# Performance work log

Hardware: AMD Instinct MI355X
Metric: run time of the kernel (lower is better)

Reference implementation:

```python
import jax, jax.numpy as jnp
import numpy as np

T, H, N, Q, C = 65536, 768, 32768, 32768, 10
MAX_LEN = 16  # max span length


def _make_spans(key, n):
    k1, k2 = jax.random.split(key)
    starts = jax.random.randint(k1, (n,), 0, T - MAX_LEN)
    lengths = jax.random.randint(k2, (n,), 1, MAX_LEN + 1)
    return jnp.stack([starts, starts + lengths], axis=1)  # [start, end)


def setup_inputs() -> dict:
    key = jax.random.key(0)
    ks = jax.random.split(key, 6)
    token_emb = jax.random.normal(ks[0], (T, H), dtype=jnp.float32)
    spans_support = _make_spans(ks[1], N)
    labels = jax.random.randint(ks[2], (N,), 0, C)
    spans_query = _make_spans(ks[3], Q)
    W_proj = jax.random.normal(ks[4], (3 * H, H), dtype=jnp.float32) * (1.0 / np.sqrt(3 * H))
    b_proj = jnp.zeros((H,), dtype=jnp.float32)
    return dict(token_emb=token_emb, spans_support=spans_support, labels=labels,
                spans_query=spans_query, W_proj=W_proj, b_proj=b_proj, n_classes=C)


def _span_embed(token_emb, spans, W, b):
    # token_emb: (T, H); spans: (n, 2) [start, end)
    s = spans[:, 0]
    e = spans[:, 1]
    # exclusive-prefix-sum trick turns per-span mean pooling into two gathers
    zero = jnp.zeros((1, token_emb.shape[1]), token_emb.dtype)
    csum = jnp.concatenate([zero, jnp.cumsum(token_emb, axis=0)], axis=0)  # (T+1, H)
    h_mean = (csum[e] - csum[s]) / (e - s).astype(token_emb.dtype)[:, None]
    feat = jnp.concatenate([token_emb[s], token_emb[e - 1], h_mean], axis=-1)  # (n, 3H)
    return jax.nn.gelu(feat @ W + b, approximate=False)  # torch nn.GELU default = erf


def _l2norm(x, eps=1e-12):
    # matches torch F.normalize: x / max(||x||, eps)
    return x / jnp.maximum(jnp.linalg.norm(x, axis=-1, keepdims=True), eps)


def reference(token_emb, spans_support, labels, spans_query, W_proj, b_proj, n_classes):
    sup = _span_embed(token_emb, spans_support, W_proj, b_proj)  # (N, H)
    qry = _span_embed(token_emb, spans_query, W_proj, b_proj)    # (Q, H)
    # prototypes = per-class mean; empty classes fall back to global mean
    sums = jax.ops.segment_sum(sup, labels, num_segments=n_classes)           # (C, H)
    counts = jax.ops.segment_sum(jnp.ones((sup.shape[0],), sup.dtype), labels,
                                 num_segments=n_classes)                       # (C,)
    gmean = sup.mean(axis=0)
    protos = jnp.where(counts[:, None] > 0,
                       sums / jnp.maximum(counts, 1.0)[:, None],
                       gmean[None, :])
    # cosine metric + constant NONE logit of 0.5
    sim = _l2norm(qry) @ _l2norm(protos).T                                     # (Q, C)
    none_logit = jnp.full((qry.shape[0], 1), 0.5, dtype=qry.dtype)
    return jnp.concatenate([sim, none_logit], axis=-1)                         # (Q, C+1)
```

## Files before the change

kernel.cpp:

```cpp
#include <hip/hip_runtime.h>
#include <stdint.h>

#define H_DIM 768
#define N_SUP 32768
#define Q_QRY 32768
#define C_CLS 10
#define M_TOT 65536
#define KG 768
#define NG 2304
#define NT 12

typedef __bf16 bf16x8 __attribute__((ext_vector_type(8)));
typedef float f32x4 __attribute__((ext_vector_type(4)));
typedef __attribute__((address_space(3))) void lds_void;
typedef const __attribute__((address_space(1))) void g_void;

__device__ __forceinline__ ushort f2bf(float f) {
  union { float f; uint32_t u; } v; v.f = f;
  uint32_t r = (v.u + 0x7FFFu + ((v.u >> 16) & 1u)) >> 16;
  return (ushort)r;
}
__device__ __forceinline__ float bf2f(ushort h) {
  union { uint32_t u; float f; } v; v.u = ((uint32_t)h) << 16; return v.f;
}
__device__ __forceinline__ float gelu_f(float x) {
  return 0.5f * x * (1.0f + erff(x * 0.70710678118654752f));
}

__global__ void cvt_kernel(const float* __restrict__ te, ushort* __restrict__ tb) {
  size_t i = (((size_t)blockIdx.x * 256) + threadIdx.x) * 8;
  float4 v0 = *(const float4*)(te + i);
  float4 v1 = *(const float4*)(te + i + 4);
  ushort4 o0, o1;
  o0.x = f2bf(v0.x); o0.y = f2bf(v0.y); o0.z = f2bf(v0.z); o0.w = f2bf(v0.w);
  o1.x = f2bf(v1.x); o1.y = f2bf(v1.y); o1.z = f2bf(v1.z); o1.w = f2bf(v1.w);
  *(ushort4*)(tb + i) = o0;
  *(ushort4*)(tb + i + 4) = o1;
}

__global__ void wt2_kernel(const float* __restrict__ W, ushort* __restrict__ Bt) {
  int idx = blockIdx.x * 256 + threadIdx.x;
  int n = idx / KG, k = idx - n * KG;
  int blk = n / H_DIM;
  int c = n - blk * H_DIM;
  Bt[idx] = f2bf(W[(size_t)(blk * H_DIM + k) * H_DIM + c]);
}

__global__ __launch_bounds__(512, 2) void gemm8(const ushort* __restrict__ A,
                                                const ushort* __restrict__ Bt,
                                                ushort* __restrict__ C) {
  __shared__ ushort lds[65536];
  char* ldsc = (char*)lds;

  int orig = blockIdx.x;
  int wg = (orig & 7) * 288 + (orig >> 3);
  int rowT = wg / 9, colT = wg - rowT * 9;
  int m0 = rowT * 256, n0 = colT * 256;

  int tid = threadIdx.x;
  int lane = tid & 63, wave = tid >> 6;
  int wr = wave >> 2, wc = wave & 3;
  int l15 = lane & 15, l4 = lane >> 4;

  int row0 = tid >> 2;
  int ss = (tid & 3) ^ ((row0 >> 1) & 3);
  size_t eA0 = (size_t)(m0 + row0) * KG + ss * 8;
  size_t eA1 = (size_t)(m0 + row0 + 128) * KG + ss * 8;
  size_t eB0 = (size_t)(n0 + row0) * KG + ss * 8;
  size_t eB1 = (size_t)(n0 + row0 + 128) * KG + ss * 8;

  int aoff[8], boff[4];
#pragma unroll
  for (int m = 0; m < 8; ++m) {
    int r = wr * 128 + m * 16 + l15;
    aoff[m] = r * 64 + ((l4 ^ ((r >> 1) & 3)) << 4);
  }
#pragma unroll
  for (int n = 0; n < 4; ++n) {
    int r = wc * 64 + n * 16 + l15;
    boff[n] = r * 64 + ((l4 ^ ((r >> 1) & 3)) << 4);
  }

  f32x4 acc[8][4];
#pragma unroll
  for (int m = 0; m < 8; ++m)
#pragma unroll
    for (int n = 0; n < 4; ++n) acc[m][n] = (f32x4){0.f, 0.f, 0.f, 0.f};

#define SLOT_A(kh, db) (ldsc + ((kh) * 2 + (db)) * 16384)
#define SLOT_B(kh, db) (ldsc + 65536 + ((kh) * 2 + (db)) * 16384)
#define STAGE_A(tk, kh, db) do { \
    char* _d = SLOT_A(kh, db) + wave * 1024; \
    size_t _k = (size_t)(tk) * 64 + (kh) * 32; \
    __builtin_amdgcn_global_load_lds((g_void*)(A + eA0 + _k), (lds_void*)_d, 16, 0, 0); \
    __builtin_amdgcn_global_load_lds((g_void*)(A + eA1 + _k), (lds_void*)(_d + 8192), 16, 0, 0); \
  } while (0)
#define STAGE_B(tk, kh, db) do { \
    char* _d = SLOT_B(kh, db) + wave * 1024; \
    size_t _k = (size_t)(tk) * 64 + (kh) * 32; \
    __builtin_amdgcn_global_load_lds((g_void*)(Bt + eB0 + _k), (lds_void*)_d, 16, 0, 0); \
    __builtin_amdgcn_global_load_lds((g_void*)(Bt + eB1 + _k), (lds_void*)(_d + 8192), 16, 0, 0); \
  } while (0)
#define LDA4(base, o) do { _Pragma("unroll") for (int m = 0; m < 4; ++m) \
    af[m] = *reinterpret_cast<const bf16x8*>((base) + aoff[(o) + m]); } while (0)
#define LDB4(base) do { _Pragma("unroll") for (int n = 0; n < 4; ++n) \
    bf[n] = *reinterpret_cast<const bf16x8*>((base) + boff[n]); } while (0)
#define MFMA_BLOCK(MB) do { _Pragma("unroll") for (int m = 0; m < 4; ++m) \
  _Pragma("unroll") for (int n = 0; n < 4; ++n) \
    acc[(MB) + m][n] = __builtin_amdgcn_mfma_f32_16x16x32_bf16(af[m], bf[n], acc[(MB) + m][n], 0, 0, 0); \
  } while (0)
#define BARX() __builtin_amdgcn_s_barrier()
#define LGKM0() asm volatile("s_waitcnt lgkmcnt(0)" ::: "memory")
#define VM8() asm volatile("s_waitcnt vmcnt(8)" ::: "memory")

  STAGE_A(0, 0, 0); STAGE_B(0, 0, 0);
  STAGE_A(0, 1, 0); STAGE_B(0, 1, 0);
  STAGE_A(1, 0, 1); STAGE_B(1, 0, 1);
  VM8();
  BARX();

  bf16x8 af[4], bf[4];
  for (int t = 0; t < NT; ++t) {
    int d = t & 1, nd = d ^ 1;
    int tk1 = (t + 1 < NT) ? t + 1 : NT - 1;
    int tk2 = (t + 2 < NT) ? t + 2 : NT - 1;
    const char* Ak0 = SLOT_A(0, d); const char* Bk0 = SLOT_B(0, d);
    const char* Ak1 = SLOT_A(1, d); const char* Bk1 = SLOT_B(1, d);
    LDA4(Ak0, 0); LDB4(Bk0);
    STAGE_A(tk1, 1, nd);
    BARX(); LGKM0();
    __builtin_amdgcn_s_setprio(1); MFMA_BLOCK(0); __builtin_amdgcn_s_setprio(0);
    BARX();
    LDA4(Ak0, 4);
    STAGE_B(tk1, 1, nd);
    BARX(); LGKM0();
    __builtin_amdgcn_s_setprio(1); MFMA_BLOCK(4); __builtin_amdgcn_s_setprio(0);
    VM8(); BARX();
    LDA4(Ak1, 0); LDB4(Bk1);
    STAGE_A(tk2, 0, d);
    BARX(); LGKM0();
    __builtin_amdgcn_s_setprio(1); MFMA_BLOCK(0); __builtin_amdgcn_s_setprio(0);
    BARX();
    LDA4(Ak1, 4);
    STAGE_B(tk2, 0, d);
    BARX(); LGKM0();
    __builtin_amdgcn_s_setprio(1); MFMA_BLOCK(4); __builtin_amdgcn_s_setprio(0);
    VM8(); BARX();
  }
  asm volatile("s_waitcnt vmcnt(0)" ::: "memory");

#pragma unroll
  for (int m = 0; m < 8; ++m)
#pragma unroll
    for (int n = 0; n < 4; ++n) {
      int col = n0 + wc * 64 + n * 16 + l15;
      size_t rb = (size_t)(m0 + wr * 128 + m * 16 + l4 * 4) * NG + col;
#pragma unroll
      for (int v = 0; v < 4; ++v)
        C[rb + (size_t)v * NG] = f2bf(acc[m][n][v]);
    }
#undef SLOT_A
#undef SLOT_B
#undef STAGE_A
#undef STAGE_B
#undef LDA4
#undef LDB4
#undef MFMA_BLOCK
}

__global__ void combine_kernel(const ushort* __restrict__ PQR, const int* __restrict__ spS,
                               const int* __restrict__ spQ, const float* __restrict__ bias,
                               ushort* __restrict__ emb) {
  int wid = (int)((((size_t)blockIdx.x * blockDim.x) + threadIdx.x) >> 6);
  int lane = threadIdx.x & 63;
  if (wid >= M_TOT) return;
  int s, e;
  if (wid < N_SUP) { s = spS[2 * wid]; e = spS[2 * wid + 1]; }
  else             { int w = wid - N_SUP; s = spQ[2 * w]; e = spQ[2 * w + 1]; }
  int len = e - s;
  float inv = 1.0f / (float)len;

  float acc0[3][4], accr[3][4];
  const ushort* Pr = PQR + (size_t)s * NG;
  const ushort* Qr = PQR + (size_t)(e - 1) * NG + 768;
#pragma unroll
  for (int c = 0; c < 3; ++c) {
    int h = c * 256 + lane * 4;
    ushort4 p = *(const ushort4*)(Pr + h);
    ushort4 q = *(const ushort4*)(Qr + h);
    acc0[c][0] = bf2f(p.x) + bf2f(q.x);
    acc0[c][1] = bf2f(p.y) + bf2f(q.y);
    acc0[c][2] = bf2f(p.z) + bf2f(q.z);
    acc0[c][3] = bf2f(p.w) + bf2f(q.w);
    accr[c][0] = accr[c][1] = accr[c][2] = accr[c][3] = 0.f;
  }
  for (int r = s; r < e; ++r) {
    const ushort* Rr = PQR + (size_t)r * NG + 1536;
#pragma unroll
    for (int c = 0; c < 3; ++c) {
      int h = c * 256 + lane * 4;
      ushort4 rv = *(const ushort4*)(Rr + h);
      accr[c][0] += bf2f(rv.x); accr[c][1] += bf2f(rv.y);
      accr[c][2] += bf2f(rv.z); accr[c][3] += bf2f(rv.w);
    }
  }
  ushort* er = emb + (size_t)wid * H_DIM;
#pragma unroll
  for (int c = 0; c < 3; ++c) {
    int h = c * 256 + lane * 4;
    float4 bv = *(const float4*)(bias + h);
    ushort4 o;
    o.x = f2bf(gelu_f(acc0[c][0] + accr[c][0] * inv + bv.x));
    o.y = f2bf(gelu_f(acc0[c][1] + accr[c][1] * inv + bv.y));
    o.z = f2bf(gelu_f(acc0[c][2] + accr[c][2] * inv + bv.z));
    o.w = f2bf(gelu_f(acc0[c][3] + accr[c][3] * inv + bv.w));
    *(ushort4*)(er + h) = o;
  }
}

__global__ void proto_accum(const ushort* __restrict__ supEmb, const int* __restrict__ labels,
                            float* __restrict__ pSum, float* __restrict__ pCnt) {
  __shared__ float ls[C_CLS * H_DIM];
  __shared__ int lc[C_CLS];
  int t = threadIdx.x;
  for (int i = t; i < C_CLS * H_DIM; i += 256) ls[i] = 0.f;
  if (t < C_CLS) lc[t] = 0;
  __syncthreads();
  int base = blockIdx.x * 128;
  for (int si = 0; si < 128; ++si) {
    int sp = base + si;
    int lab = labels[sp];
    const ushort* er = supEmb + (size_t)sp * H_DIM;
#pragma unroll
    for (int j = 0; j < 3; ++j) {
      int c = t + j * 256;
      ls[lab * H_DIM + c] += bf2f(er[c]);
    }
    if (t == 0) lc[lab]++;
  }
  __syncthreads();
  for (int i = t; i < C_CLS * H_DIM; i += 256) atomicAdd(&pSum[i], ls[i]);
  if (t < C_CLS) atomicAdd(&pCnt[t], (float)lc[t]);
}

__global__ void proto_norm(const float* __restrict__ pSum, const float* __restrict__ pCnt,
                           float* __restrict__ pN) {
  __shared__ float red[4];
  int t = threadIdx.x, lane = t & 63, wave = t >> 6;
  for (int c = 0; c < C_CLS; ++c) {
    float cnt = pCnt[c];
    float x[3];
#pragma unroll
    for (int j = 0; j < 3; ++j) {
      int h = t + j * 256;
      float v;
      if (cnt > 0.5f) v = pSum[c * H_DIM + h] / cnt;
      else {
        float gs = 0.f;
        for (int cc = 0; cc < C_CLS; ++cc) gs += pSum[cc * H_DIM + h];
        v = gs / (float)N_SUP;
      }
      x[j] = v;
    }
    float ss = x[0] * x[0] + x[1] * x[1] + x[2] * x[2];
#pragma unroll
    for (int o = 32; o; o >>= 1) ss += __shfl_xor(ss, o);
    if (lane == 0) red[wave] = ss;
    __syncthreads();
    float tot = red[0] + red[1] + red[2] + red[3];
    float inv = 1.0f / fmaxf(sqrtf(tot), 1e-12f);
#pragma unroll
    for (int j = 0; j < 3; ++j) pN[c * H_DIM + t + j * 256] = x[j] * inv;
    __syncthreads();
  }
}

__global__ void sim_kernel(const ushort* __restrict__ emb, const float* __restrict__ pN,
                           float* __restrict__ out) {
  __shared__ float lp[C_CLS * H_DIM];
  int t = threadIdx.x;
  for (int i = t; i < C_CLS * H_DIM; i += 256) lp[i] = pN[i];
  __syncthreads();
  int lane = t & 63, wave = t >> 6;
  for (int row = blockIdx.x * 4 + wave; row < Q_QRY; row += gridDim.x * 4) {
    const ushort* qr = emb + (size_t)(N_SUP + row) * H_DIM;
    float dot[C_CLS] = {0, 0, 0, 0, 0, 0, 0, 0, 0, 0};
    float sq = 0.f;
#pragma unroll
    for (int j = 0; j < 12; ++j) {
      float v = bf2f(qr[lane + 64 * j]);
      sq += v * v;
#pragma unroll
      for (int p = 0; p < C_CLS; ++p) dot[p] += v * lp[p * H_DIM + lane + 64 * j];
    }
#pragma unroll
    for (int o = 32; o; o >>= 1) {
      sq += __shfl_xor(sq, o);
#pragma unroll
      for (int p = 0; p < C_CLS; ++p) dot[p] += __shfl_xor(dot[p], o);
    }
    if (lane == 0) {
      float inv = 1.0f / fmaxf(sqrtf(sq), 1e-12f);
      float* o = out + (size_t)row * (C_CLS + 1);
      o[0] = dot[0] * inv; o[1] = dot[1] * inv; o[2] = dot[2] * inv;
      o[3] = dot[3] * inv; o[4] = dot[4] * inv; o[5] = dot[5] * inv;
      o[6] = dot[6] * inv; o[7] = dot[7] * inv; o[8] = dot[8] * inv;
      o[9] = dot[9] * inv; o[10] = 0.5f;
    }
  }
}

extern "C" void kernel_launch(void* const* d_in, const int* in_sizes, int n_in,
                              void* d_out, int out_size, void* d_ws, size_t ws_size,
                              hipStream_t stream) {
  const float* token_emb = (const float*)d_in[0];
  const int*   spansS    = (const int*)d_in[1];
  const int*   labels    = (const int*)d_in[2];
  const int*   spansQ    = (const int*)d_in[3];
  const float* W         = (const float*)d_in[4];
  const float* b         = (const float*)d_in[5];
  float* out = (float*)d_out;

  char* ws = (char*)d_ws;
  size_t pqrB = (size_t)M_TOT * NG * 2;
  size_t embB = (size_t)M_TOT * H_DIM * 2;
  size_t wtB  = (size_t)NG * KG * 2;
  ushort* PQR  = (ushort*)ws;
  ushort* tebf = (ushort*)(ws + pqrB);
  ushort* emb  = tebf;
  ushort* Bt   = (ushort*)(ws + pqrB + embB);
  float*  pSum = (float*)(ws + pqrB + embB + wtB);
  float*  pCnt = pSum + C_CLS * H_DIM;
  float*  pN   = pCnt + 64;

  hipMemsetAsync(pSum, 0, (C_CLS * H_DIM + 64) * sizeof(float), stream);
  cvt_kernel<<<24576, 256, 0, stream>>>(token_emb, tebf);
  wt2_kernel<<<6912, 256, 0, stream>>>(W, Bt);
  gemm8<<<2304, 512, 0, stream>>>(tebf, Bt, PQR);
  combine_kernel<<<16384, 256, 0, stream>>>(PQR, spansS, spansQ, b, emb);
  proto_accum<<<N_SUP / 128, 256, 0, stream>>>(emb, labels, pSum, pCnt);
  proto_norm<<<1, 256, 0, stream>>>(pSum, pCnt, pN);
  sim_kernel<<<512, 256, 0, stream>>>(emb, pN, out);
}
```

Baseline: 630.1 us.

## Make GEMM persistent per row tile, looping over column tiles with cross-pass prefetch

```diff
diff --git a/kernel.cpp b/kernel.cpp
--- a/kernel.cpp
+++ b/kernel.cpp
@@ -9,6 +9,7 @@
 #define KG 768
 #define NG 2304
 #define NT 12
+#define NPASS 9
 
 typedef __bf16 bf16x8 __attribute__((ext_vector_type(8)));
 typedef float f32x4 __attribute__((ext_vector_type(4)));
@@ -46,16 +47,13 @@
   Bt[idx] = f2bf(W[(size_t)(blk * H_DIM + k) * H_DIM + c]);
 }
 
-__global__ __launch_bounds__(512, 2) void gemm8(const ushort* __restrict__ A,
-                                                const ushort* __restrict__ Bt,
-                                                ushort* __restrict__ C) {
+__global__ __launch_bounds__(512, 2) void gemm_p(const ushort* __restrict__ A,
+                                                 const ushort* __restrict__ Bt,
+                                                 ushort* __restrict__ C) {
   __shared__ ushort lds[65536];
   char* ldsc = (char*)lds;
 
-  int orig = blockIdx.x;
-  int wg = (orig & 7) * 288 + (orig >> 3);
-  int rowT = wg / 9, colT = wg - rowT * 9;
-  int m0 = rowT * 256, n0 = colT * 256;
+  int m0 = blockIdx.x * 256;
 
   int tid = threadIdx.x;
   int lane = tid & 63, wave = tid >> 6;
@@ -66,8 +64,8 @@
   int ss = (tid & 3) ^ ((row0 >> 1) & 3);
   size_t eA0 = (size_t)(m0 + row0) * KG + ss * 8;
   size_t eA1 = (size_t)(m0 + row0 + 128) * KG + ss * 8;
-  size_t eB0 = (size_t)(n0 + row0) * KG + ss * 8;
-  size_t eB1 = (size_t)(n0 + row0 + 128) * KG + ss * 8;
+  size_t eB0 = (size_t)row0 * KG + ss * 8;
+  size_t eB1 = (size_t)(row0 + 128) * KG + ss * 8;
 
   int aoff[8], boff[4];
 #pragma unroll
@@ -89,15 +87,15 @@
 
 #define SLOT_A(kh, db) (ldsc + ((kh) * 2 + (db)) * 16384)
 #define SLOT_B(kh, db) (ldsc + 65536 + ((kh) * 2 + (db)) * 16384)
-#define STAGE_A(tk, kh, db) do { \
+#define SA(kOff, kh, db) do { \
     char* _d = SLOT_A(kh, db) + wave * 1024; \
-    size_t _k = (size_t)(tk) * 64 + (kh) * 32; \
+    size_t _k = (size_t)(kOff) + (kh) * 32; \
     __builtin_amdgcn_global_load_lds((g_void*)(A + eA0 + _k), (lds_void*)_d, 16, 0, 0); \
     __builtin_amdgcn_global_load_lds((g_void*)(A + eA1 + _k), (lds_void*)(_d + 8192), 16, 0, 0); \
   } while (0)
-#define STAGE_B(tk, kh, db) do { \
+#define SB(cOff, kOff, kh, db) do { \
     char* _d = SLOT_B(kh, db) + wave * 1024; \
-    size_t _k = (size_t)(tk) * 64 + (kh) * 32; \
+    size_t _k = (size_t)(cOff) + (kOff) + (kh) * 32; \
     __builtin_amdgcn_global_load_lds((g_void*)(Bt + eB0 + _k), (lds_void*)_d, 16, 0, 0); \
     __builtin_amdgcn_global_load_lds((g_void*)(Bt + eB1 + _k), (lds_void*)(_d + 8192), 16, 0, 0); \
   } while (0)
@@ -107,62 +105,78 @@
     bf[n] = *reinterpret_cast<const bf16x8*>((base) + boff[n]); } while (0)
 #define MFMA_BLOCK(MB) do { _Pragma("unroll") for (int m = 0; m < 4; ++m) \
   _Pragma("unroll") for (int n = 0; n < 4; ++n) \
-    acc[(MB) + m][n] = __builtin_amdgcn_mfma_f32_16x16x32_bf16(af[m], bf[n], acc[(MB) + m][n], 0, 0, 0); \
+    acc[(MB) + m][n] = __builtin_amdgcn_mfma_f32_16x16x32_bf16(bf[n], af[m], acc[(MB) + m][n], 0, 0, 0); \
   } while (0)
 #define BARX() __builtin_amdgcn_s_barrier()
 #define LGKM0() asm volatile("s_waitcnt lgkmcnt(0)" ::: "memory")
-#define VM8() asm volatile("s_waitcnt vmcnt(8)" ::: "memory")
-
-  STAGE_A(0, 0, 0); STAGE_B(0, 0, 0);
-  STAGE_A(0, 1, 0); STAGE_B(0, 1, 0);
-  STAGE_A(1, 0, 1); STAGE_B(1, 0, 1);
-  VM8();
+#define VM4() asm volatile("s_waitcnt vmcnt(4)" ::: "memory")
+
+  SA(0, 0, 0);  SB(0, 0, 0, 0);
+  SA(0, 1, 0);  SB(0, 0, 1, 0);
+  SA(64, 0, 1); SB(0, 64, 0, 1);
+  VM4();
   BARX();
 
   bf16x8 af[4], bf[4];
-  for (int t = 0; t < NT; ++t) {
-    int d = t & 1, nd = d ^ 1;
-    int tk1 = (t + 1 < NT) ? t + 1 : NT - 1;
-    int tk2 = (t + 2 < NT) ? t + 2 : NT - 1;
-    const char* Ak0 = SLOT_A(0, d); const char* Bk0 = SLOT_B(0, d);
-    const char* Ak1 = SLOT_A(1, d); const char* Bk1 = SLOT_B(1, d);
-    LDA4(Ak0, 0); LDB4(Bk0);
-    STAGE_A(tk1, 1, nd);
-    BARX(); LGKM0();
-    __builtin_amdgcn_s_setprio(1); MFMA_BLOCK(0); __builtin_amdgcn_s_setprio(0);
-    BARX();
-    LDA4(Ak0, 4);
-    STAGE_B(tk1, 1, nd);
-    BARX(); LGKM0();
-    __builtin_amdgcn_s_setprio(1); MFMA_BLOCK(4); __builtin_amdgcn_s_setprio(0);
-    VM8(); BARX();
-    LDA4(Ak1, 0); LDB4(Bk1);
-    STAGE_A(tk2, 0, d);
-    BARX(); LGKM0();
-    __builtin_amdgcn_s_setprio(1); MFMA_BLOCK(0); __builtin_amdgcn_s_setprio(0);
-    BARX();
-    LDA4(Ak1, 4);
-    STAGE_B(tk2, 0, d);
-    BARX(); LGKM0();
-    __builtin_amdgcn_s_setprio(1); MFMA_BLOCK(4); __builtin_amdgcn_s_setprio(0);
-    VM8(); BARX();
+  for (int p = 0; p < NPASS; ++p) {
+    for (int t = 0; t < NT; ++t) {
+      int d = t & 1, nd = d ^ 1;
+      int tt1, ct1, tt2, ct2;
+      if (t < 11) { tt1 = t + 1; ct1 = p; } else { tt1 = 0; ct1 = p + 1; }
+      if (t < 10) { tt2 = t + 2; ct2 = p; } else { tt2 = t - 10; ct2 = p + 1; }
+      if (ct1 >= NPASS) { ct1 = NPASS - 1; tt1 = NT - 1; }
+      if (ct2 >= NPASS) { ct2 = NPASS - 1; tt2 = NT - 1; }
+      size_t cO1 = (size_t)ct1 * 256 * KG;
+      size_t cO2 = (size_t)ct2 * 256 * KG;
+      const char* Ak0 = SLOT_A(0, d); const char* Bk0 = SLOT_B(0, d);
+      const char* Ak1 = SLOT_A(1, d); const char* Bk1 = SLOT_B(1, d);
+      LDA4(Ak0, 0); LDB4(Bk0);
+      SA(tt1 * 64, 1, nd);
+      BARX(); LGKM0();
+      __builtin_amdgcn_s_setprio(1); MFMA_BLOCK(0); __builtin_amdgcn_s_setprio(0);
+      BARX();
+      LDA4(Ak0, 4);
+      SB(cO1, tt1 * 64, 1, nd);
+      BARX(); LGKM0();
+      __builtin_amdgcn_s_setprio(1); MFMA_BLOCK(4); __builtin_amdgcn_s_setprio(0);
+      BARX();
+      LDA4(Ak1, 0); LDB4(Bk1);
+      SA(tt2 * 64, 0, d);
+      BARX(); LGKM0();
+      __builtin_amdgcn_s_setprio(1); MFMA_BLOCK(0); __builtin_amdgcn_s_setprio(0);
+      BARX();
+      LDA4(Ak1, 4);
+      SB(cO2, tt2 * 64, 0, d);
+      BARX(); LGKM0();
+      __builtin_amdgcn_s_setprio(1); MFMA_BLOCK(4); __builtin_amdgcn_s_setprio(0);
+      VM4(); BARX();
+    }
+    {
+      int n0 = p * 256;
+#pragma unroll
+      for (int m = 0; m < 8; ++m) {
+        int row = m0 + wr * 128 + m * 16 + l15;
+#pragma unroll
+        for (int n = 0; n < 4; ++n) {
+          int col = n0 + wc * 64 + n * 16 + l4 * 4;
+          uint32_t lo, hi;
+          asm("v_cvt_pk_bf16_f32 %0, %1, %2" : "=v"(lo) : "v"(acc[m][n][0]), "v"(acc[m][n][1]));
+          asm("v_cvt_pk_bf16_f32 %0, %1, %2" : "=v"(hi) : "v"(acc[m][n][2]), "v"(acc[m][n][3]));
+          uint2 val; val.x = lo; val.y = hi;
+          *reinterpret_cast<uint2*>(C + (size_t)row * NG + col) = val;
+        }
+      }
+#pragma unroll
+      for (int m = 0; m < 8; ++m)
+#pragma unroll
+        for (int n = 0; n < 4; ++n) acc[m][n] = (f32x4){0.f, 0.f, 0.f, 0.f};
+    }
   }
   asm volatile("s_waitcnt vmcnt(0)" ::: "memory");
-
-#pragma unroll
-  for (int m = 0; m < 8; ++m)
-#pragma unroll
-    for (int n = 0; n < 4; ++n) {
-      int col = n0 + wc * 64 + n * 16 + l15;
-      size_t rb = (size_t)(m0 + wr * 128 + m * 16 + l4 * 4) * NG + col;
-#pragma unroll
-      for (int v = 0; v < 4; ++v)
-        C[rb + (size_t)v * NG] = f2bf(acc[m][n][v]);
-    }
 #undef SLOT_A
 #undef SLOT_B
-#undef STAGE_A
-#undef STAGE_B
+#undef SA
+#undef SB
 #undef LDA4
 #undef LDB4
 #undef MFMA_BLOCK
@@ -336,7 +350,7 @@
   hipMemsetAsync(pSum, 0, (C_CLS * H_DIM + 64) * sizeof(float), stream);
   cvt_kernel<<<24576, 256, 0, stream>>>(token_emb, tebf);
   wt2_kernel<<<6912, 256, 0, stream>>>(W, Bt);
-  gemm8<<<2304, 512, 0, stream>>>(tebf, Bt, PQR);
+  gemm_p<<<256, 512, 0, stream>>>(tebf, Bt, PQR);
   combine_kernel<<<16384, 256, 0, stream>>>(PQR, spansS, spansQ, b, emb);
   proto_accum<<<N_SUP / 128, 256, 0, stream>>>(emb, labels, pSum, pCnt);
   proto_norm<<<1, 256, 0, stream>>>(pSum, pCnt, pN);
```

Measured after the change: 673.3 us. 1.07x slower.

## Split GEMM output into P/Q/R planes, sort spans by start, restructure MFMA pipeline

Applied to the files above, without the earlier changes.

```diff
diff --git a/kernel.cpp b/kernel.cpp
--- a/kernel.cpp
+++ b/kernel.cpp
@@ -7,8 +7,8 @@
 #define C_CLS 10
 #define M_TOT 65536
 #define KG 768
-#define NG 2304
 #define NT 12
+#define NBUCK 1024
 
 typedef __bf16 bf16x8 __attribute__((ext_vector_type(8)));
 typedef float f32x4 __attribute__((ext_vector_type(4)));
@@ -46,16 +46,59 @@
   Bt[idx] = f2bf(W[(size_t)(blk * H_DIM + k) * H_DIM + c]);
 }
 
+__global__ void hist_kernel(const int* __restrict__ spS, const int* __restrict__ spQ,
+                            int* __restrict__ hist) {
+  __shared__ int lh[NBUCK];
+  int t = threadIdx.x;
+  for (int i = t; i < NBUCK; i += 256) lh[i] = 0;
+  __syncthreads();
+  for (int i = blockIdx.x * 256 + t; i < M_TOT; i += gridDim.x * 256) {
+    int s = (i < N_SUP) ? spS[2 * i] : spQ[2 * (i - N_SUP)];
+    atomicAdd(&lh[s >> 6], 1);
+  }
+  __syncthreads();
+  for (int i = t; i < NBUCK; i += 256) if (lh[i]) atomicAdd(&hist[i], lh[i]);
+}
+
+__global__ void prefix_kernel(const int* __restrict__ hist, int* __restrict__ cursor) {
+  __shared__ int tmp[NBUCK];
+  int t = threadIdx.x;
+  int v = hist[t];
+  tmp[t] = v;
+  __syncthreads();
+  for (int off = 1; off < NBUCK; off <<= 1) {
+    int add = (t >= off) ? tmp[t - off] : 0;
+    __syncthreads();
+    tmp[t] += add;
+    __syncthreads();
+  }
+  cursor[t] = tmp[t] - v;
+}
+
+__global__ void scatter_kernel(const int* __restrict__ spS, const int* __restrict__ spQ,
+                               int* __restrict__ cursor, int2* __restrict__ sorted) {
+  for (int i = blockIdx.x * 256 + threadIdx.x; i < M_TOT; i += gridDim.x * 256) {
+    int s, e;
+    if (i < N_SUP) { s = spS[2 * i]; e = spS[2 * i + 1]; }
+    else           { int w = i - N_SUP; s = spQ[2 * w]; e = spQ[2 * w + 1]; }
+    int pos = atomicAdd(&cursor[s >> 6], 1);
+    int2 rec; rec.x = s; rec.y = (i << 5) | (e - s);
+    sorted[pos] = rec;
+  }
+}
+
 __global__ __launch_bounds__(512, 2) void gemm8(const ushort* __restrict__ A,
                                                 const ushort* __restrict__ Bt,
-                                                ushort* __restrict__ C) {
+                                                ushort* __restrict__ Pp,
+                                                ushort* __restrict__ Qp,
+                                                ushort* __restrict__ Rp) {
   __shared__ ushort lds[65536];
   char* ldsc = (char*)lds;
 
   int orig = blockIdx.x;
   int wg = (orig & 7) * 288 + (orig >> 3);
   int rowT = wg / 9, colT = wg - rowT * 9;
-  int m0 = rowT * 256, n0 = colT * 256;
+  int m0 = rowT * 256;
 
   int tid = threadIdx.x;
   int lane = tid & 63, wave = tid >> 6;
@@ -66,8 +109,8 @@
   int ss = (tid & 3) ^ ((row0 >> 1) & 3);
   size_t eA0 = (size_t)(m0 + row0) * KG + ss * 8;
   size_t eA1 = (size_t)(m0 + row0 + 128) * KG + ss * 8;
-  size_t eB0 = (size_t)(n0 + row0) * KG + ss * 8;
-  size_t eB1 = (size_t)(n0 + row0 + 128) * KG + ss * 8;
+  size_t eB0 = (size_t)(colT * 256 + row0) * KG + ss * 8;
+  size_t eB1 = (size_t)(colT * 256 + row0 + 128) * KG + ss * 8;
 
   int aoff[8], boff[4];
 #pragma unroll
@@ -89,100 +132,95 @@
 
 #define SLOT_A(kh, db) (ldsc + ((kh) * 2 + (db)) * 16384)
 #define SLOT_B(kh, db) (ldsc + 65536 + ((kh) * 2 + (db)) * 16384)
-#define STAGE_A(tk, kh, db) do { \
-    char* _d = SLOT_A(kh, db) + wave * 1024; \
-    size_t _k = (size_t)(tk) * 64 + (kh) * 32; \
-    __builtin_amdgcn_global_load_lds((g_void*)(A + eA0 + _k), (lds_void*)_d, 16, 0, 0); \
-    __builtin_amdgcn_global_load_lds((g_void*)(A + eA1 + _k), (lds_void*)(_d + 8192), 16, 0, 0); \
+#define SAB(kOff, kh, db) do { \
+    char* _da = SLOT_A(kh, db) + wave * 1024; \
+    char* _db = SLOT_B(kh, db) + wave * 1024; \
+    size_t _k = (size_t)(kOff) + (kh) * 32; \
+    __builtin_amdgcn_global_load_lds((g_void*)(A + eA0 + _k), (lds_void*)_da, 16, 0, 0); \
+    __builtin_amdgcn_global_load_lds((g_void*)(A + eA1 + _k), (lds_void*)(_da + 8192), 16, 0, 0); \
+    __builtin_amdgcn_global_load_lds((g_void*)(Bt + eB0 + _k), (lds_void*)_db, 16, 0, 0); \
+    __builtin_amdgcn_global_load_lds((g_void*)(Bt + eB1 + _k), (lds_void*)(_db + 8192), 16, 0, 0); \
   } while (0)
-#define STAGE_B(tk, kh, db) do { \
-    char* _d = SLOT_B(kh, db) + wave * 1024; \
-    size_t _k = (size_t)(tk) * 64 + (kh) * 32; \
-    __builtin_amdgcn_global_load_lds((g_void*)(Bt + eB0 + _k), (lds_void*)_d, 16, 0, 0); \
-    __builtin_amdgcn_global_load_lds((g_void*)(Bt + eB1 + _k), (lds_void*)(_d + 8192), 16, 0, 0); \
-  } while (0)
-#define LDA4(base, o) do { _Pragma("unroll") for (int m = 0; m < 4; ++m) \
-    af[m] = *reinterpret_cast<const bf16x8*>((base) + aoff[(o) + m]); } while (0)
+#define LDA8(base) do { _Pragma("unroll") for (int m = 0; m < 8; ++m) \
+    af[m] = *reinterpret_cast<const bf16x8*>((base) + aoff[m]); } while (0)
 #define LDB4(base) do { _Pragma("unroll") for (int n = 0; n < 4; ++n) \
     bf[n] = *reinterpret_cast<const bf16x8*>((base) + boff[n]); } while (0)
-#define MFMA_BLOCK(MB) do { _Pragma("unroll") for (int m = 0; m < 4; ++m) \
+#define MFMA32() do { _Pragma("unroll") for (int m = 0; m < 8; ++m) \
   _Pragma("unroll") for (int n = 0; n < 4; ++n) \
-    acc[(MB) + m][n] = __builtin_amdgcn_mfma_f32_16x16x32_bf16(af[m], bf[n], acc[(MB) + m][n], 0, 0, 0); \
+    acc[m][n] = __builtin_amdgcn_mfma_f32_16x16x32_bf16(bf[n], af[m], acc[m][n], 0, 0, 0); \
   } while (0)
 #define BARX() __builtin_amdgcn_s_barrier()
 #define LGKM0() asm volatile("s_waitcnt lgkmcnt(0)" ::: "memory")
 #define VM8() asm volatile("s_waitcnt vmcnt(8)" ::: "memory")
 
-  STAGE_A(0, 0, 0); STAGE_B(0, 0, 0);
-  STAGE_A(0, 1, 0); STAGE_B(0, 1, 0);
-  STAGE_A(1, 0, 1); STAGE_B(1, 0, 1);
+  SAB(0, 0, 0);
+  SAB(0, 1, 0);
+  SAB(64, 0, 1);
   VM8();
   BARX();
 
-  bf16x8 af[4], bf[4];
+  bf16x8 af[8], bf[4];
   for (int t = 0; t < NT; ++t) {
     int d = t & 1, nd = d ^ 1;
-    int tk1 = (t + 1 < NT) ? t + 1 : NT - 1;
-    int tk2 = (t + 2 < NT) ? t + 2 : NT - 1;
-    const char* Ak0 = SLOT_A(0, d); const char* Bk0 = SLOT_B(0, d);
-    const char* Ak1 = SLOT_A(1, d); const char* Bk1 = SLOT_B(1, d);
-    LDA4(Ak0, 0); LDB4(Bk0);
-    STAGE_A(tk1, 1, nd);
+    int k1 = ((t + 1 < NT) ? t + 1 : NT - 1) * 64;
+    int k2 = ((t + 2 < NT) ? t + 2 : NT - 1) * 64;
+    LDA8(SLOT_A(0, d)); LDB4(SLOT_B(0, d));
+    SAB(k1, 1, nd);
     BARX(); LGKM0();
-    __builtin_amdgcn_s_setprio(1); MFMA_BLOCK(0); __builtin_amdgcn_s_setprio(0);
+    __builtin_amdgcn_s_setprio(1); MFMA32(); __builtin_amdgcn_s_setprio(0);
+    VM8();
     BARX();
-    LDA4(Ak0, 4);
-    STAGE_B(tk1, 1, nd);
+    LDA8(SLOT_A(1, d)); LDB4(SLOT_B(1, d));
+    SAB(k2, 0, d);
     BARX(); LGKM0();
-    __builtin_amdgcn_s_setprio(1); MFMA_BLOCK(4); __builtin_amdgcn_s_setprio(0);
-    VM8(); BARX();
-    LDA4(Ak1, 0); LDB4(Bk1);
-    STAGE_A(tk2, 0, d);
-    BARX(); LGKM0();
-    __builtin_amdgcn_s_setprio(1); MFMA_BLOCK(0); __builtin_amdgcn_s_setprio(0);
+    __builtin_amdgcn_s_setprio(1); MFMA32(); __builtin_amdgcn_s_setprio(0);
+    VM8();
     BARX();
-    LDA4(Ak1, 4);
-    STAGE_B(tk2, 0, d);
-    BARX(); LGKM0();
-    __builtin_amdgcn_s_setprio(1); MFMA_BLOCK(4); __builtin_amdgcn_s_setprio(0);
-    VM8(); BARX();
   }
   asm volatile("s_waitcnt vmcnt(0)" ::: "memory");
 
-#pragma unroll
-  for (int m = 0; m < 8; ++m)
-#pragma unroll
-    for (int n = 0; n < 4; ++n) {
-      int col = n0 + wc * 64 + n * 16 + l15;
-      size_t rb = (size_t)(m0 + wr * 128 + m * 16 + l4 * 4) * NG + col;
-#pragma unroll
-      for (int v = 0; v < 4; ++v)
-        C[rb + (size_t)v * NG] = f2bf(acc[m][n][v]);
-    }
+  {
+    int plane = colT / 3;
+    int pcol0 = colT * 256 - plane * 768;
+    ushort* base = (plane == 0) ? Pp : ((plane == 1) ? Qp : Rp);
+#pragma unroll
+    for (int m = 0; m < 8; ++m) {
+      int row = m0 + wr * 128 + m * 16 + l15;
+#pragma unroll
+      for (int n = 0; n < 4; ++n) {
+        int col = pcol0 + wc * 64 + n * 16 + l4 * 4;
+        uint32_t lo, hi;
+        asm("v_cvt_pk_bf16_f32 %0, %1, %2" : "=v"(lo) : "v"(acc[m][n][0]), "v"(acc[m][n][1]));
+        asm("v_cvt_pk_bf16_f32 %0, %1, %2" : "=v"(hi) : "v"(acc[m][n][2]), "v"(acc[m][n][3]));
+        uint2 val; val.x = lo; val.y = hi;
+        *reinterpret_cast<uint2*>(base + (size_t)row * H_DIM + col) = val;
+      }
+    }
+  }
 #undef SLOT_A
 #undef SLOT_B
-#undef STAGE_A
-#undef STAGE_B
-#undef LDA4
+#undef SAB
+#undef LDA8
 #undef LDB4
-#undef MFMA_BLOCK
-}
-
-__global__ void combine_kernel(const ushort* __restrict__ PQR, const int* __restrict__ spS,
-                               const int* __restrict__ spQ, const float* __restrict__ bias,
-                               ushort* __restrict__ emb) {
+#undef MFMA32
+}
+
+__global__ void combine2(const ushort* __restrict__ Pp, const ushort* __restrict__ Qp,
+                         const ushort* __restrict__ Rp, const int2* __restrict__ sorted,
+                         const float* __restrict__ bias, ushort* __restrict__ emb) {
   int wid = (int)((((size_t)blockIdx.x * blockDim.x) + threadIdx.x) >> 6);
   int lane = threadIdx.x & 63;
   if (wid >= M_TOT) return;
-  int s, e;
-  if (wid < N_SUP) { s = spS[2 * wid]; e = spS[2 * wid + 1]; }
-  else             { int w = wid - N_SUP; s = spQ[2 * w]; e = spQ[2 * w + 1]; }
-  int len = e - s;
+  int2 rec = sorted[wid];
+  int s = rec.x;
+  int len = rec.y & 31;
+  int orig = rec.y >> 5;
+  int e = s + len;
   float inv = 1.0f / (float)len;
 
   float acc0[3][4], accr[3][4];
-  const ushort* Pr = PQR + (size_t)s * NG;
-  const ushort* Qr = PQR + (size_t)(e - 1) * NG + 768;
+  const ushort* Pr = Pp + (size_t)s * H_DIM;
+  const ushort* Qr = Qp + (size_t)(e - 1) * H_DIM;
 #pragma unroll
   for (int c = 0; c < 3; ++c) {
     int h = c * 256 + lane * 4;
@@ -195,7 +233,7 @@
     accr[c][0] = accr[c][1] = accr[c][2] = accr[c][3] = 0.f;
   }
   for (int r = s; r < e; ++r) {
-    const ushort* Rr = PQR + (size_t)r * NG + 1536;
+    const ushort* Rr = Rp + (size_t)r * H_DIM;
 #pragma unroll
     for (int c = 0; c < 3; ++c) {
       int h = c * 256 + lane * 4;
@@ -204,7 +242,7 @@
       accr[c][2] += bf2f(rv.z); accr[c][3] += bf2f(rv.w);
     }
   }
-  ushort* er = emb + (size_t)wid * H_DIM;
+  ushort* er = emb + (size_t)orig * H_DIM;
 #pragma unroll
   for (int c = 0; c < 3; ++c) {
     int h = c * 256 + lane * 4;
@@ -322,22 +360,30 @@
   float* out = (float*)d_out;
 
   char* ws = (char*)d_ws;
-  size_t pqrB = (size_t)M_TOT * NG * 2;
-  size_t embB = (size_t)M_TOT * H_DIM * 2;
-  size_t wtB  = (size_t)NG * KG * 2;
-  ushort* PQR  = (ushort*)ws;
-  ushort* tebf = (ushort*)(ws + pqrB);
+  size_t planeB = (size_t)M_TOT * H_DIM * 2;
+  ushort* Pp   = (ushort*)ws;
+  ushort* Qp   = (ushort*)(ws + planeB);
+  ushort* Rp   = (ushort*)(ws + 2 * planeB);
+  ushort* tebf = (ushort*)(ws + 3 * planeB);
   ushort* emb  = tebf;
-  ushort* Bt   = (ushort*)(ws + pqrB + embB);
-  float*  pSum = (float*)(ws + pqrB + embB + wtB);
+  ushort* Bt   = (ushort*)(ws + 4 * planeB);
+  char*   tail = ws + 4 * planeB + (size_t)2304 * KG * 2;
+  float*  pSum = (float*)tail;
   float*  pCnt = pSum + C_CLS * H_DIM;
   float*  pN   = pCnt + 64;
+  int*    hist = (int*)(pN + C_CLS * H_DIM);
+  int*    cursor = hist + NBUCK;
+  int2*   sorted = (int2*)(cursor + NBUCK);
 
   hipMemsetAsync(pSum, 0, (C_CLS * H_DIM + 64) * sizeof(float), stream);
+  hipMemsetAsync(hist, 0, NBUCK * sizeof(int), stream);
   cvt_kernel<<<24576, 256, 0, stream>>>(token_emb, tebf);
   wt2_kernel<<<6912, 256, 0, stream>>>(W, Bt);
-  gemm8<<<2304, 512, 0, stream>>>(tebf, Bt, PQR);
-  combine_kernel<<<16384, 256, 0, stream>>>(PQR, spansS, spansQ, b, emb);
+  hist_kernel<<<64, 256, 0, stream>>>(spansS, spansQ, hist);
+  prefix_kernel<<<1, NBUCK, 0, stream>>>(hist, cursor);
+  scatter_kernel<<<64, 256, 0, stream>>>(spansS, spansQ, cursor, sorted);
+  gemm8<<<2304, 512, 0, stream>>>(tebf, Bt, Pp, Qp, Rp);
+  combine2<<<16384, 256, 0, stream>>>(Pp, Qp, Rp, sorted, b, emb);
   proto_accum<<<N_SUP / 128, 256, 0, stream>>>(emb, labels, pSum, pCnt);
   proto_norm<<<1, 256, 0, stream>>>(pSum, pCnt, pN);
   sim_kernel<<<512, 256, 0, stream>>>(emb, pN, out);
```

New measurement: 676.7 us. 7.4% more time.

## Fuse span combine into proto/sim kernels, bucket-sort spans, split GEMM output planes

Applied to the files above, without the earlier changes.

```diff
diff --git a/kernel.cpp b/kernel.cpp
--- a/kernel.cpp
+++ b/kernel.cpp
@@ -7,8 +7,8 @@
 #define C_CLS 10
 #define M_TOT 65536
 #define KG 768
-#define NG 2304
 #define NT 12
+#define NBUCK 1024
 
 typedef __bf16 bf16x8 __attribute__((ext_vector_type(8)));
 typedef float f32x4 __attribute__((ext_vector_type(4)));
@@ -27,28 +27,98 @@
   return 0.5f * x * (1.0f + erff(x * 0.70710678118654752f));
 }
 
-__global__ void cvt_kernel(const float* __restrict__ te, ushort* __restrict__ tb) {
-  size_t i = (((size_t)blockIdx.x * 256) + threadIdx.x) * 8;
-  float4 v0 = *(const float4*)(te + i);
-  float4 v1 = *(const float4*)(te + i + 4);
-  ushort4 o0, o1;
-  o0.x = f2bf(v0.x); o0.y = f2bf(v0.y); o0.z = f2bf(v0.z); o0.w = f2bf(v0.w);
-  o1.x = f2bf(v1.x); o1.y = f2bf(v1.y); o1.z = f2bf(v1.z); o1.w = f2bf(v1.w);
-  *(ushort4*)(tb + i) = o0;
-  *(ushort4*)(tb + i + 4) = o1;
-}
-
-__global__ void wt2_kernel(const float* __restrict__ W, ushort* __restrict__ Bt) {
-  int idx = blockIdx.x * 256 + threadIdx.x;
-  int n = idx / KG, k = idx - n * KG;
-  int blk = n / H_DIM;
-  int c = n - blk * H_DIM;
-  Bt[idx] = f2bf(W[(size_t)(blk * H_DIM + k) * H_DIM + c]);
+__global__ void prep_kernel(const float* __restrict__ te, const float* __restrict__ W,
+                            const int* __restrict__ spS, const int* __restrict__ spQ,
+                            ushort* __restrict__ tb, ushort* __restrict__ Bt,
+                            int* __restrict__ histS, int* __restrict__ histQ) {
+  int b = blockIdx.x, t = threadIdx.x;
+  if (b < 24576) {
+    size_t i = (((size_t)b * 256) + t) * 8;
+    float4 v0 = *(const float4*)(te + i);
+    float4 v1 = *(const float4*)(te + i + 4);
+    ushort4 o0, o1;
+    o0.x = f2bf(v0.x); o0.y = f2bf(v0.y); o0.z = f2bf(v0.z); o0.w = f2bf(v0.w);
+    o1.x = f2bf(v1.x); o1.y = f2bf(v1.y); o1.z = f2bf(v1.z); o1.w = f2bf(v1.w);
+    *(ushort4*)(tb + i) = o0;
+    *(ushort4*)(tb + i + 4) = o1;
+  } else if (b < 31488) {
+    int idx = (b - 24576) * 256 + t;
+    int n = idx / KG, k = idx - n * KG;
+    int blk = n / H_DIM;
+    int c = n - blk * H_DIM;
+    Bt[idx] = f2bf(W[(size_t)(blk * H_DIM + k) * H_DIM + c]);
+  } else {
+    __shared__ int lhS[NBUCK], lhQ[NBUCK];
+    for (int i = t; i < NBUCK; i += 256) { lhS[i] = 0; lhQ[i] = 0; }
+    __syncthreads();
+    int b0 = b - 31488;
+    for (int i = b0 * 256 + t; i < N_SUP; i += 64 * 256) {
+      atomicAdd(&lhS[spS[2 * i] >> 6], 1);
+      atomicAdd(&lhQ[spQ[2 * i] >> 6], 1);
+    }
+    __syncthreads();
+    for (int i = t; i < NBUCK; i += 256) {
+      if (lhS[i]) atomicAdd(&histS[i], lhS[i]);
+      if (lhQ[i]) atomicAdd(&histQ[i], lhQ[i]);
+    }
+  }
+}
+
+__global__ void prefix2_kernel(const int* __restrict__ histS, const int* __restrict__ histQ,
+                               int* __restrict__ curS, int* __restrict__ curQ) {
+  __shared__ int tmp[NBUCK];
+  int t = threadIdx.x;
+  {
+    int v = histS[t];
+    tmp[t] = v;
+    __syncthreads();
+    for (int off = 1; off < NBUCK; off <<= 1) {
+      int add = (t >= off) ? tmp[t - off] : 0;
+      __syncthreads();
+      tmp[t] += add;
+      __syncthreads();
+    }
+    curS[t] = tmp[t] - v;
+    __syncthreads();
+  }
+  {
+    int v = histQ[t];
+    tmp[t] = v;
+    __syncthreads();
+    for (int off = 1; off < NBUCK; off <<= 1) {
+      int add = (t >= off) ? tmp[t - off] : 0;
+      __syncthreads();
+      tmp[t] += add;
+      __syncthreads();
+    }
+    curQ[t] = tmp[t] - v;
+  }
+}
+
+__global__ void scatter2_kernel(const int* __restrict__ spS, const int* __restrict__ spQ,
+                                int* __restrict__ curS, int* __restrict__ curQ,
+                                int2* __restrict__ sortedS, int2* __restrict__ sortedQ) {
+  for (int i = blockIdx.x * 256 + threadIdx.x; i < N_SUP; i += gridDim.x * 256) {
+    {
+      int s = spS[2 * i], e = spS[2 * i + 1];
+      int pos = atomicAdd(&curS[s >> 6], 1);
+      int2 rec; rec.x = s; rec.y = (i << 5) | (e - s);
+      sortedS[pos] = rec;
+    }
+    {
+      int s = spQ[2 * i], e = spQ[2 * i + 1];
+      int pos = atomicAdd(&curQ[s >> 6], 1);
+      int2 rec; rec.x = s; rec.y = (i << 5) | (e - s);
+      sortedQ[pos] = rec;
+    }
+  }
 }
 
 __global__ __launch_bounds__(512, 2) void gemm8(const ushort* __restrict__ A,
                                                 const ushort* __restrict__ Bt,
-                                                ushort* __restrict__ C) {
+                                                ushort* __restrict__ Pp,
+                                                ushort* __restrict__ Qp,
+                                                ushort* __restrict__ Rp) {
   __shared__ ushort lds[65536];
   char* ldsc = (char*)lds;
 
@@ -107,7 +177,7 @@
     bf[n] = *reinterpret_cast<const bf16x8*>((base) + boff[n]); } while (0)
 #define MFMA_BLOCK(MB) do { _Pragma("unroll") for (int m = 0; m < 4; ++m) \
   _Pragma("unroll") for (int n = 0; n < 4; ++n) \
-    acc[(MB) + m][n] = __builtin_amdgcn_mfma_f32_16x16x32_bf16(af[m], bf[n], acc[(MB) + m][n], 0, 0, 0); \
+    acc[(MB) + m][n] = __builtin_amdgcn_mfma_f32_16x16x32_bf16(bf[n], af[m], acc[(MB) + m][n], 0, 0, 0); \
   } while (0)
 #define BARX() __builtin_amdgcn_s_barrier()
 #define LGKM0() asm volatile("s_waitcnt lgkmcnt(0)" ::: "memory")
@@ -149,16 +219,24 @@
   }
   asm volatile("s_waitcnt vmcnt(0)" ::: "memory");
 
-#pragma unroll
-  for (int m = 0; m < 8; ++m)
-#pragma unroll
-    for (int n = 0; n < 4; ++n) {
-      int col = n0 + wc * 64 + n * 16 + l15;
-      size_t rb = (size_t)(m0 + wr * 128 + m * 16 + l4 * 4) * NG + col;
-#pragma unroll
-      for (int v = 0; v < 4; ++v)
-        C[rb + (size_t)v * NG] = f2bf(acc[m][n][v]);
-    }
+  {
+    int plane = colT / 3;
+    int pcol0 = colT * 256 - plane * 768;
+    ushort* base = (plane == 0) ? Pp : ((plane == 1) ? Qp : Rp);
+#pragma unroll
+    for (int m = 0; m < 8; ++m) {
+      int row = m0 + wr * 128 + m * 16 + l15;
+#pragma unroll
+      for (int n = 0; n < 4; ++n) {
+        int col = pcol0 + wc * 64 + n * 16 + l4 * 4;
+        uint32_t lo, hi;
+        asm("v_cvt_pk_bf16_f32 %0, %1, %2" : "=v"(lo) : "v"(acc[m][n][0]), "v"(acc[m][n][1]));
+        asm("v_cvt_pk_bf16_f32 %0, %1, %2" : "=v"(hi) : "v"(acc[m][n][2]), "v"(acc[m][n][3]));
+        uint2 val; val.x = lo; val.y = hi;
+        *reinterpret_cast<uint2*>(base + (size_t)row * H_DIM + col) = val;
+      }
+    }
+  }
 #undef SLOT_A
 #undef SLOT_B
 #undef STAGE_A
@@ -168,21 +246,16 @@
 #undef MFMA_BLOCK
 }
 
-__global__ void combine_kernel(const ushort* __restrict__ PQR, const int* __restrict__ spS,
-                               const int* __restrict__ spQ, const float* __restrict__ bias,
-                               ushort* __restrict__ emb) {
-  int wid = (int)((((size_t)blockIdx.x * blockDim.x) + threadIdx.x) >> 6);
-  int lane = threadIdx.x & 63;
-  if (wid >= M_TOT) return;
-  int s, e;
-  if (wid < N_SUP) { s = spS[2 * wid]; e = spS[2 * wid + 1]; }
-  else             { int w = wid - N_SUP; s = spQ[2 * w]; e = spQ[2 * w + 1]; }
-  int len = e - s;
+__device__ __forceinline__ void span_embed(const ushort* __restrict__ Pp,
+                                           const ushort* __restrict__ Qp,
+                                           const ushort* __restrict__ Rp,
+                                           const float* __restrict__ bias,
+                                           int s, int len, int lane, float x[3][4]) {
+  int e = s + len;
   float inv = 1.0f / (float)len;
-
   float acc0[3][4], accr[3][4];
-  const ushort* Pr = PQR + (size_t)s * NG;
-  const ushort* Qr = PQR + (size_t)(e - 1) * NG + 768;
+  const ushort* Pr = Pp + (size_t)s * H_DIM;
+  const ushort* Qr = Qp + (size_t)(e - 1) * H_DIM;
 #pragma unroll
   for (int c = 0; c < 3; ++c) {
     int h = c * 256 + lane * 4;
@@ -195,7 +268,7 @@
     accr[c][0] = accr[c][1] = accr[c][2] = accr[c][3] = 0.f;
   }
   for (int r = s; r < e; ++r) {
-    const ushort* Rr = PQR + (size_t)r * NG + 1536;
+    const ushort* Rr = Rp + (size_t)r * H_DIM;
 #pragma unroll
     for (int c = 0; c < 3; ++c) {
       int h = c * 256 + lane * 4;
@@ -204,39 +277,47 @@
       accr[c][2] += bf2f(rv.z); accr[c][3] += bf2f(rv.w);
     }
   }
-  ushort* er = emb + (size_t)wid * H_DIM;
 #pragma unroll
   for (int c = 0; c < 3; ++c) {
     int h = c * 256 + lane * 4;
     float4 bv = *(const float4*)(bias + h);
-    ushort4 o;
-    o.x = f2bf(gelu_f(acc0[c][0] + accr[c][0] * inv + bv.x));
-    o.y = f2bf(gelu_f(acc0[c][1] + accr[c][1] * inv + bv.y));
-    o.z = f2bf(gelu_f(acc0[c][2] + accr[c][2] * inv + bv.z));
-    o.w = f2bf(gelu_f(acc0[c][3] + accr[c][3] * inv + bv.w));
-    *(ushort4*)(er + h) = o;
-  }
-}
-
-__global__ void proto_accum(const ushort* __restrict__ supEmb, const int* __restrict__ labels,
-                            float* __restrict__ pSum, float* __restrict__ pCnt) {
+    x[c][0] = gelu_f(acc0[c][0] + accr[c][0] * inv + bv.x);
+    x[c][1] = gelu_f(acc0[c][1] + accr[c][1] * inv + bv.y);
+    x[c][2] = gelu_f(acc0[c][2] + accr[c][2] * inv + bv.z);
+    x[c][3] = gelu_f(acc0[c][3] + accr[c][3] * inv + bv.w);
+  }
+}
+
+__global__ __launch_bounds__(256) void combine_sup(const ushort* __restrict__ Pp,
+                                                   const ushort* __restrict__ Qp,
+                                                   const ushort* __restrict__ Rp,
+                                                   const int2* __restrict__ sortedS,
+                                                   const int* __restrict__ labels,
+                                                   const float* __restrict__ bias,
+                                                   float* __restrict__ pSum,
+                                                   float* __restrict__ pCnt) {
   __shared__ float ls[C_CLS * H_DIM];
   __shared__ int lc[C_CLS];
-  int t = threadIdx.x;
+  int t = threadIdx.x, lane = t & 63, wave = t >> 6;
   for (int i = t; i < C_CLS * H_DIM; i += 256) ls[i] = 0.f;
   if (t < C_CLS) lc[t] = 0;
   __syncthreads();
-  int base = blockIdx.x * 128;
-  for (int si = 0; si < 128; ++si) {
-    int sp = base + si;
-    int lab = labels[sp];
-    const ushort* er = supEmb + (size_t)sp * H_DIM;
-#pragma unroll
-    for (int j = 0; j < 3; ++j) {
-      int c = t + j * 256;
-      ls[lab * H_DIM + c] += bf2f(er[c]);
-    }
-    if (t == 0) lc[lab]++;
+  for (int si = wave; si < 128; si += 4) {
+    int2 rec = sortedS[blockIdx.x * 128 + si];
+    int s = rec.x, len = rec.y & 31, orig = rec.y >> 5;
+    float x[3][4];
+    span_embed(Pp, Qp, Rp, bias, s, len, lane, x);
+    int lab = labels[orig];
+    float* base = &ls[lab * H_DIM];
+#pragma unroll
+    for (int c = 0; c < 3; ++c) {
+      int h = c * 256 + lane * 4;
+      atomicAdd(&base[h], x[c][0]);
+      atomicAdd(&base[h + 1], x[c][1]);
+      atomicAdd(&base[h + 2], x[c][2]);
+      atomicAdd(&base[h + 3], x[c][3]);
+    }
+    if (lane == 0) atomicAdd(&lc[lab], 1);
   }
   __syncthreads();
   for (int i = t; i < C_CLS * H_DIM; i += 256) atomicAdd(&pSum[i], ls[i]);
@@ -275,38 +356,48 @@
   }
 }
 
-__global__ void sim_kernel(const ushort* __restrict__ emb, const float* __restrict__ pN,
-                           float* __restrict__ out) {
+__global__ __launch_bounds__(256) void combine_qry_sim(const ushort* __restrict__ Pp,
+                                                       const ushort* __restrict__ Qp,
+                                                       const ushort* __restrict__ Rp,
+                                                       const int2* __restrict__ sortedQ,
+                                                       const float* __restrict__ bias,
+                                                       const float* __restrict__ pN,
+                                                       float* __restrict__ out) {
   __shared__ float lp[C_CLS * H_DIM];
-  int t = threadIdx.x;
+  int t = threadIdx.x, lane = t & 63, wave = t >> 6;
   for (int i = t; i < C_CLS * H_DIM; i += 256) lp[i] = pN[i];
   __syncthreads();
-  int lane = t & 63, wave = t >> 6;
-  for (int row = blockIdx.x * 4 + wave; row < Q_QRY; row += gridDim.x * 4) {
-    const ushort* qr = emb + (size_t)(N_SUP + row) * H_DIM;
-    float dot[C_CLS] = {0, 0, 0, 0, 0, 0, 0, 0, 0, 0};
-    float sq = 0.f;
-#pragma unroll
-    for (int j = 0; j < 12; ++j) {
-      float v = bf2f(qr[lane + 64 * j]);
-      sq += v * v;
-#pragma unroll
-      for (int p = 0; p < C_CLS; ++p) dot[p] += v * lp[p * H_DIM + lane + 64 * j];
-    }
-#pragma unroll
-    for (int o = 32; o; o >>= 1) {
-      sq += __shfl_xor(sq, o);
-#pragma unroll
-      for (int p = 0; p < C_CLS; ++p) dot[p] += __shfl_xor(dot[p], o);
-    }
-    if (lane == 0) {
-      float inv = 1.0f / fmaxf(sqrtf(sq), 1e-12f);
-      float* o = out + (size_t)row * (C_CLS + 1);
-      o[0] = dot[0] * inv; o[1] = dot[1] * inv; o[2] = dot[2] * inv;
-      o[3] = dot[3] * inv; o[4] = dot[4] * inv; o[5] = dot[5] * inv;
-      o[6] = dot[6] * inv; o[7] = dot[7] * inv; o[8] = dot[8] * inv;
-      o[9] = dot[9] * inv; o[10] = 0.5f;
-    }
+  int2 rec = sortedQ[blockIdx.x * 4 + wave];
+  int s = rec.x, len = rec.y & 31, orig = rec.y >> 5;
+  float x[3][4];
+  span_embed(Pp, Qp, Rp, bias, s, len, lane, x);
+  float sq = 0.f;
+  float dot[C_CLS];
+#pragma unroll
+  for (int p = 0; p < C_CLS; ++p) dot[p] = 0.f;
+#pragma unroll
+  for (int c = 0; c < 3; ++c) {
+    int h = c * 256 + lane * 4;
+    sq += x[c][0] * x[c][0] + x[c][1] * x[c][1] + x[c][2] * x[c][2] + x[c][3] * x[c][3];
+#pragma unroll
+    for (int p = 0; p < C_CLS; ++p) {
+      float4 pv = *(const float4*)(lp + p * H_DIM + h);
+      dot[p] += x[c][0] * pv.x + x[c][1] * pv.y + x[c][2] * pv.z + x[c][3] * pv.w;
+    }
+  }
+#pragma unroll
+  for (int o = 32; o; o >>= 1) {
+    sq += __shfl_xor(sq, o);
+#pragma unroll
+    for (int p = 0; p < C_CLS; ++p) dot[p] += __shfl_xor(dot[p], o);
+  }
+  if (lane == 0) {
+    float inv = 1.0f / fmaxf(sqrtf(sq), 1e-12f);
+    float* o = out + (size_t)orig * (C_CLS + 1);
+    o[0] = dot[0] * inv; o[1] = dot[1] * inv; o[2] = dot[2] * inv;
+    o[3] = dot[3] * inv; o[4] = dot[4] * inv; o[5] = dot[5] * inv;
+    o[6] = dot[6] * inv; o[7] = dot[7] * inv; o[8] = dot[8] * inv;
+    o[9] = dot[9] * inv; o[10] = 0.5f;
   }
 }
 
@@ -322,23 +413,30 @@
   float* out = (float*)d_out;
 
   char* ws = (char*)d_ws;
-  size_t pqrB = (size_t)M_TOT * NG * 2;
-  size_t embB = (size_t)M_TOT * H_DIM * 2;
-  size_t wtB  = (size_t)NG * KG * 2;
-  ushort* PQR  = (ushort*)ws;
-  ushort* tebf = (ushort*)(ws + pqrB);
-  ushort* emb  = tebf;
-  ushort* Bt   = (ushort*)(ws + pqrB + embB);
-  float*  pSum = (float*)(ws + pqrB + embB + wtB);
+  size_t planeB = (size_t)M_TOT * H_DIM * 2;
+  ushort* Pp   = (ushort*)ws;
+  ushort* Qp   = (ushort*)(ws + planeB);
+  ushort* Rp   = (ushort*)(ws + 2 * planeB);
+  ushort* tebf = (ushort*)(ws + 3 * planeB);
+  ushort* Bt   = (ushort*)(ws + 4 * planeB);
+  char*   tail = ws + 4 * planeB + (size_t)2304 * KG * 2;
+  float*  pSum = (float*)tail;
   float*  pCnt = pSum + C_CLS * H_DIM;
   float*  pN   = pCnt + 64;
+  int*    histS = (int*)(pN + C_CLS * H_DIM);
+  int*    histQ = histS + NBUCK;
+  int*    curS  = histQ + NBUCK;
+  int*    curQ  = curS + NBUCK;
+  int2*   sortedS = (int2*)(curQ + NBUCK);
+  int2*   sortedQ = sortedS + N_SUP;
 
   hipMemsetAsync(pSum, 0, (C_CLS * H_DIM + 64) * sizeof(float), stream);
-  cvt_kernel<<<24576, 256, 0, stream>>>(token_emb, tebf);
-  wt2_kernel<<<6912, 256, 0, stream>>>(W, Bt);
-  gemm8<<<2304, 512, 0, stream>>>(tebf, Bt, PQR);
-  combine_kernel<<<16384, 256, 0, stream>>>(PQR, spansS, spansQ, b, emb);
-  proto_accum<<<N_SUP / 128, 256, 0, stream>>>(emb, labels, pSum, pCnt);
+  hipMemsetAsync(histS, 0, 2 * NBUCK * sizeof(int), stream);
+  prep_kernel<<<31552, 256, 0, stream>>>(token_emb, W, spansS, spansQ, tebf, Bt, histS, histQ);
+  prefix2_kernel<<<1, NBUCK, 0, stream>>>(histS, histQ, curS, curQ);
+  scatter2_kernel<<<64, 256, 0, stream>>>(spansS, spansQ, curS, curQ, sortedS, sortedQ);
+  gemm8<<<2304, 512, 0, stream>>>(tebf, Bt, Pp, Qp, Rp);
+  combine_sup<<<N_SUP / 128, 256, 0, stream>>>(Pp, Qp, Rp, sortedS, labels, b, pSum, pCnt);
   proto_norm<<<1, 256, 0, stream>>>(pSum, pCnt, pN);
-  sim_kernel<<<512, 256, 0, stream>>>(emb, pN, out);
-}
+  combine_qry_sim<<<Q_QRY / 4, 256, 0, stream>>>(Pp, Qp, Rp, sortedQ, b, pN, out);
+}
```

Result: slower. 716.5 us (+13.7%).
